# Kernel tuning notes

Measured on AMD Instinct MI355X. Metric: run time of the kernel, lower is better.

The kernel has to match this reference:

```python
import jax, jax.numpy as jnp
import numpy as np
from jax import lax

B, N, C = 4, 16384, 384  # C = 2*dim
DIM = C // 2
HH = WW = 128


def setup_inputs() -> dict:
    key = jax.random.key(0)
    ks = jax.random.split(key, 5)
    x = jax.random.normal(ks[0], (B, N, C), dtype=jnp.float32)
    conv_w = jax.random.normal(ks[1], (DIM, DIM, 4, 4), dtype=jnp.float32) * (1.0 / np.sqrt(DIM * 16))
    conv_b = jax.random.normal(ks[2], (DIM,), dtype=jnp.float32) * 0.02
    ln_w = jnp.ones((C,), dtype=jnp.float32)
    ln_b = jnp.zeros((C,), dtype=jnp.float32)
    proj_w = jax.random.normal(ks[3], (C, C), dtype=jnp.float32) * (1.0 / np.sqrt(C))
    proj_b = jax.random.normal(ks[4], (C,), dtype=jnp.float32) * 0.02
    return {"x": x, "conv_w": conv_w, "conv_b": conv_b, "ln_w": ln_w,
            "ln_b": ln_b, "proj_w": proj_w, "proj_b": proj_b, "H": HH, "W": WW}


def _csb_forward(x, conv_w, conv_b, ln_w, ln_b, proj_w, proj_b, H, W):
    Bb, Nn, Cc = x.shape
    d = Cc // 2
    x1 = x[..., :d]   # [B, N, d]
    x2 = x[..., d:]   # [B, N, d]

    # --- SpatialCorrection ---
    img = jnp.transpose(x2, (0, 2, 1)).reshape(Bb, d, H, W)  # NCHW
    y = lax.conv_general_dilated(img, conv_w, window_strides=(4, 4),
                                 padding='VALID',
                                 dimension_numbers=('NCHW', 'OIHW', 'NCHW'))
    y = y + conv_b[None, :, None, None]
    x2c = y.reshape(Bb, d, Nn // 16)                          # [B, d, M]
    gate = jax.nn.sigmoid(jnp.einsum('bnd,bdm->bnm', x1, x2c))  # [B, N, M]
    sp = jnp.einsum('bnm,bdm->bnd', gate, x2c)                 # [B, N, d]

    # --- ChannelCorrection ---
    att = jax.nn.softmax(jnp.einsum('bnd,bne->bde', x1, x2), axis=-2)  # [B, d, d], softmax over dim=-2
    ch = jnp.einsum('bnd,bde->bne', x2, att)                   # [B, N, d]

    # --- concat + LN + proj ---
    cat = jnp.concatenate([sp, ch], axis=-1)                   # [B, N, 2d]
    mu = jnp.mean(cat, axis=-1, keepdims=True)
    var = jnp.mean(jnp.square(cat - mu), axis=-1, keepdims=True)
    ln = (cat - mu) * lax.rsqrt(var + 1e-5) * ln_w + ln_b
    out = jnp.einsum('bnc,oc->bno', ln, proj_w) + proj_b
    return jnp.transpose(out, (0, 2, 1))                       # [B, 2d, N]


def reference(x, conv_w, conv_b, ln_w, ln_b, proj_w, proj_b, H, W):
    return _csb_forward(x, conv_w, conv_b, ln_w, ln_b, proj_w, proj_b, H, W)
```

## Files before the change

### kernel.cpp

```cpp
#include <hip/hip_runtime.h>

#define BB 4
#define NN 16384
#define CC 384
#define DD 192
#define MM 1024

typedef __attribute__((ext_vector_type(8))) short short8;
typedef __attribute__((ext_vector_type(4))) float f32x4;
typedef unsigned short u16;

__device__ __forceinline__ float4 ld4(const float* p) { return *reinterpret_cast<const float4*>(p); }

__device__ __forceinline__ u16 bf16r(float f) {
    unsigned int u = __float_as_uint(f);
    return (u16)((u + 0x7FFFu + ((u >> 16) & 1u)) >> 16);
}
__device__ __forceinline__ unsigned int pk2(float a, float b) {
    return (unsigned int)bf16r(a) | ((unsigned int)bf16r(b) << 16);
}
__device__ __forceinline__ short8 as_s8(uint4 v) {
    union { uint4 u; short8 s; } x; x.u = v; return x.s;
}
__device__ __forceinline__ f32x4 mfma16(short8 a, short8 b, f32x4 c) {
    return __builtin_amdgcn_mfma_f32_16x16x32_bf16(a, b, c, 0, 0, 0);
}
__device__ __forceinline__ void gload16(const void* g, void* l) {
    __builtin_amdgcn_global_load_lds(
        (const __attribute__((address_space(1))) void*)g,
        (__attribute__((address_space(3))) void*)l, 16, 0, 0);
}

__global__ __launch_bounds__(256) void k_prep(const float* __restrict__ pw, u16* __restrict__ pwb)
{
    int i = blockIdx.x * 256 + threadIdx.x;
    float4 v = ld4(&pw[i * 4]);
    uint2 o; o.x = pk2(v.x, v.y); o.y = pk2(v.z, v.w);
    reinterpret_cast<uint2*>(pwb)[i] = o;
}

__global__ __launch_bounds__(256) void k_prepw(const float* __restrict__ cw, u16* __restrict__ cwb)
{
    int idx = blockIdx.x * 256 + threadIdx.x;
    int k8 = idx / 192, o = idx % 192;
    int px = k8 / 24;
    int i0 = (k8 % 24) * 8;
    float f[8];
    #pragma unroll
    for (int e = 0; e < 8; ++e) f[e] = cw[(size_t)(o * 192 + i0 + e) * 16 + px];
    uint4 v = make_uint4(pk2(f[0], f[1]), pk2(f[2], f[3]), pk2(f[4], f[5]), pk2(f[6], f[7]));
    reinterpret_cast<uint4*>(cwb)[idx] = v;
}

__global__ __launch_bounds__(256) void k_conv(const float* __restrict__ x,
                                              const u16* __restrict__ cwb,
                                              float* __restrict__ Cp2)
{
    const int bid = blockIdx.x;
    const int s = bid >> 8, pt = bid & 255;
    const int b = pt >> 6;
    const int m0 = (pt & 63) * 16;
    const int P0 = pt * 16;
    const int t = threadIdx.x;
    const int l = t & 63, w = t >> 6;
    const int l15 = l & 15, l4 = l >> 4;
    const int o0 = w * 48;

    const int m = m0 + l15;
    const int ph = m >> 5, pw_ = m & 31;
    const float* xp = x + ((size_t)(b * NN) + ph * 512 + pw_ * 4) * CC + DD;

    f32x4 acc[3];
    #pragma unroll
    for (int ft = 0; ft < 3; ++ft) acc[ft] = (f32x4){0.f, 0.f, 0.f, 0.f};

    for (int kt = 0; kt < 48; ++kt) {
        const int px = s * 8 + kt / 6;
        const int i0 = (kt % 6) * 32;
        const int kh = px >> 2, kw = px & 3;
        const float* src = xp + (size_t)(kh * 128 + kw) * CC + i0 + l4 * 8;
        float4 v0 = ld4(src), v1 = ld4(src + 4);
        short8 av = as_s8(make_uint4(pk2(v0.x, v0.y), pk2(v0.z, v0.w), pk2(v1.x, v1.y), pk2(v1.z, v1.w)));
        const int k8g = px * 24 + (kt % 6) * 4 + l4;
        #pragma unroll
        for (int ft = 0; ft < 3; ++ft) {
            int o = o0 + ft * 16 + l15;
            short8 bv = as_s8(*reinterpret_cast<const uint4*>(cwb + (size_t)(k8g * 192 + o) * 8));
            acc[ft] = mfma16(av, bv, acc[ft]);
        }
    }
    #pragma unroll
    for (int ft = 0; ft < 3; ++ft)
        #pragma unroll
        for (int i = 0; i < 4; ++i)
            Cp2[(size_t)(s * 4096 + P0 + l4 * 4 + i) * 192 + o0 + ft * 16 + l15] = acc[ft][i];
}

__global__ __launch_bounds__(256) void k_convred(const float* __restrict__ Cp2,
                                                 const float* __restrict__ cb,
                                                 u16* __restrict__ x2cT,
                                                 u16* __restrict__ x2cM)
{
    __shared__ u16 T[64 * 194];
    const int bid = blockIdx.x;
    const int b = bid >> 4, mc = bid & 15;
    const int P0 = b * 1024 + mc * 64;
    const int t = threadIdx.x;
    #pragma unroll
    for (int j = 0; j < 12; ++j) {
        int idx = j * 256 + t;
        int row = idx / 48, c4 = idx % 48;
        float4 v0 = ld4(&Cp2[(size_t)(P0 + row) * 192 + c4 * 4]);
        float4 v1 = ld4(&Cp2[(size_t)(4096 + P0 + row) * 192 + c4 * 4]);
        float4 bb = ld4(&cb[c4 * 4]);
        float r0 = v0.x + v1.x + bb.x, r1 = v0.y + v1.y + bb.y;
        float r2 = v0.z + v1.z + bb.z, r3 = v0.w + v1.w + bb.w;
        u16 h0 = bf16r(r0), h1 = bf16r(r1), h2 = bf16r(r2), h3 = bf16r(r3);
        uint2 ov; ov.x = (unsigned int)h0 | ((unsigned int)h1 << 16);
        ov.y = (unsigned int)h2 | ((unsigned int)h3 << 16);
        *reinterpret_cast<uint2*>(x2cT + (size_t)(P0 + row) * 192 + c4 * 4) = ov;
        T[row * 194 + c4 * 4 + 0] = h0; T[row * 194 + c4 * 4 + 1] = h1;
        T[row * 194 + c4 * 4 + 2] = h2; T[row * 194 + c4 * 4 + 3] = h3;
    }
    __syncthreads();
    #pragma unroll
    for (int j = 0; j < 6; ++j) {
        int u = j * 256 + t;
        int o = u >> 3, m8 = (u & 7) * 8;
        unsigned int pk[4];
        #pragma unroll
        for (int q = 0; q < 4; ++q) {
            u16 a = T[(m8 + q * 2) * 194 + o];
            u16 c = T[(m8 + q * 2 + 1) * 194 + o];
            pk[q] = (unsigned int)a | ((unsigned int)c << 16);
        }
        *reinterpret_cast<uint4*>(x2cM + ((size_t)(b * DD + o) * MM) + mc * 64 + m8) =
            make_uint4(pk[0], pk[1], pk[2], pk[3]);
    }
}

__global__ __launch_bounds__(512) void k_S(const float* __restrict__ x, float* __restrict__ Sp,
                                           int KS, int nkt)
{
    __shared__ char LS[384 * 128];
    const int bid = blockIdx.x;
    const int b = bid / KS, ks = bid % KS;
    const int n0 = ks * (NN / KS);
    const int t = threadIdx.x;
    const int l = t & 63, w = t >> 6;
    const int rg = w >> 2, cs = w & 3;
    const int l15 = l & 15, l4 = l >> 4, key = (l15 & 7) << 4;

    const int c0 = (t & 127) * 3;
    const int krow = t >> 7;

    f32x4 acc[6][3];
    #pragma unroll
    for (int dt = 0; dt < 6; ++dt)
        #pragma unroll
        for (int et = 0; et < 3; ++et) acc[dt][et] = (f32x4){0.f, 0.f, 0.f, 0.f};

    for (int kt = 0; kt < nkt; ++kt) {
        __syncthreads();
        #pragma unroll
        for (int i = 0; i < 8; ++i) {
            int k = i * 4 + krow;
            const float* src = &x[(size_t)(b * NN + n0 + kt * 32 + k) * CC + c0];
            #pragma unroll
            for (int j = 0; j < 3; ++j) {
                int c = c0 + j;
                float v = src[j];
                u16 hi = bf16r(v);
                float hif = __uint_as_float(((unsigned int)hi) << 16);
                u16 lo = bf16r(v - hif);
                int base = c * 128;
                int ck = (c & 7) << 4;
                *reinterpret_cast<u16*>(LS + base + ((k * 2) ^ ck)) = hi;
                *reinterpret_cast<u16*>(LS + base + ((64 + k * 2) ^ ck)) = lo;
            }
        }
        __syncthreads();
        short8 bf[3][2];
        #pragma unroll
        for (int et = 0; et < 3; ++et) {
            int c = 192 + cs * 48 + et * 16 + l15;
            #pragma unroll
            for (int hl = 0; hl < 2; ++hl)
                bf[et][hl] = *reinterpret_cast<const short8*>(LS + c * 128 + ((hl * 64 + l4 * 16) ^ key));
        }
        #pragma unroll
        for (int dt = 0; dt < 6; ++dt) {
            int c = rg * 96 + dt * 16 + l15;
            short8 ah = *reinterpret_cast<const short8*>(LS + c * 128 + ((l4 * 16) ^ key));
            short8 al = *reinterpret_cast<const short8*>(LS + c * 128 + ((64 + l4 * 16) ^ key));
            #pragma unroll
            for (int et = 0; et < 3; ++et) {
                acc[dt][et] = mfma16(ah, bf[et][0], acc[dt][et]);
                acc[dt][et] = mfma16(ah, bf[et][1], acc[dt][et]);
                acc[dt][et] = mfma16(al, bf[et][0], acc[dt][et]);
            }
        }
    }
    float* dst = Sp + (size_t)(ks * BB + b) * 36864;
    #pragma unroll
    for (int dt = 0; dt < 6; ++dt)
        #pragma unroll
        for (int et = 0; et < 3; ++et) {
            int e = cs * 48 + et * 16 + l15;
            #pragma unroll
            for (int i = 0; i < 4; ++i) {
                int d = rg * 96 + dt * 16 + l4 * 4 + i;
                dst[d * 192 + e] = acc[dt][et][i];
            }
        }
}

__global__ __launch_bounds__(256) void k_sreduce(const float* __restrict__ Sp, float* __restrict__ S, int KS)
{
    int idx = blockIdx.x * 256 + threadIdx.x;
    int b = idx / 36864, de = idx % 36864;
    float s = 0.f;
    for (int p = 0; p < KS; ++p) s += Sp[(size_t)(p * BB + b) * 36864 + de];
    S[(size_t)b * 36864 + de] = s;
}

__global__ __launch_bounds__(64) void k_softmax(const float* __restrict__ S, u16* __restrict__ attT)
{
    const int bid = blockIdx.x;
    const int b = bid / 192, e = bid % 192;
    const int l = threadIdx.x;
    const float* Sb = S + (size_t)b * 36864 + e;
    float v0 = Sb[(size_t)(l * 3 + 0) * 192];
    float v1 = Sb[(size_t)(l * 3 + 1) * 192];
    float v2 = Sb[(size_t)(l * 3 + 2) * 192];
    float m = fmaxf(fmaxf(v0, v1), v2);
    #pragma unroll
    for (int s = 1; s < 64; s <<= 1) m = fmaxf(m, __shfl_xor(m, s, 64));
    v0 = __expf(v0 - m); v1 = __expf(v1 - m); v2 = __expf(v2 - m);
    float sum = v0 + v1 + v2;
    #pragma unroll
    for (int s = 1; s < 64; s <<= 1) sum += __shfl_xor(sum, s, 64);
    float inv = __fdividef(1.f, sum);
    u16* dst = attT + (size_t)b * 36864 + (size_t)e * 192 + l * 3;
    dst[0] = bf16r(v0 * inv); dst[1] = bf16r(v1 * inv); dst[2] = bf16r(v2 * inv);
}

#define KG_CT(p) ((p) * 24576)
#define KG_CM(p) ((p) * 24576 + 12288)
#define KG_GT 49152

__global__ __launch_bounds__(512, 2) void k_gate(
    const float* __restrict__ x, const u16* __restrict__ x2cT,
    const u16* __restrict__ x2cMp, const u16* __restrict__ attT,
    u16* __restrict__ cat, int half)
{
    __shared__ alignas(16) char LB[53248];
    const int t = threadIdx.x;
    const int l = t & 63, w = t >> 6;
    const int rg = w >> 1, cs = w & 1;
    const int b = blockIdx.x >> 7;
    const int nloc = (blockIdx.x & 127) << 6;
    const int n0 = half * 8192 + nloc;
    const int l15 = l & 15, l4 = l >> 4, key = (l15 & 7) << 4;
    const int key3 = (l15 & 3) << 4;
    const size_t xrow0 = (size_t)(b * NN + n0) * CC;
    const char* cbase = (const char*)x2cT;

    int goff[3], gmul[3];
    #pragma unroll
    for (int it = 0; it < 3; ++it) {
        int q = it * 8192 + w * 1024 + l * 16;
        if (q < 12288) {
            int m = q / 384, c = q % 384;
            goff[it] = b * 393216 + m * 384 + (c ^ ((m & 7) << 4));
            gmul[it] = 12288;
        } else {
            int qp = q - 12288;
            int r = qp >> 7, o = qp & 127;
            int op = o ^ ((r & 7) << 4);
            int d = r * 2 + (op >> 6);
            int m = (op & 63) >> 1;
            goff[it] = 1572864 + b * 393216 + d * 2048 + m * 2;
            gmul[it] = 64;
        }
    }
    (void)x2cMp;

    short8 ax1[6];
    {
        int row = rg * 16 + l15;
        const float* src = &x[xrow0 + (size_t)row * CC + l4 * 8];
        #pragma unroll
        for (int k = 0; k < 6; ++k) {
            float4 v0 = ld4(src + k * 32), v1 = ld4(src + k * 32 + 4);
            ax1[k] = as_s8(make_uint4(pk2(v0.x, v0.y), pk2(v0.z, v0.w), pk2(v1.x, v1.y), pk2(v1.z, v1.w)));
        }
    }

    #pragma unroll
    for (int it = 0; it < 3; ++it)
        gload16(cbase + goff[it], LB + it * 8192 + w * 1024);
    __syncthreads();

    f32x4 spa[6];
    #pragma unroll
    for (int nt = 0; nt < 6; ++nt) spa[nt] = (f32x4){0.f, 0.f, 0.f, 0.f};

    int p = 0;
    for (int mc = 0; mc < 32; ++mc) {
        if (mc < 31) {
            const int pn = p ^ 1;
            #pragma unroll
            for (int it = 0; it < 3; ++it)
                gload16(cbase + goff[it] + (mc + 1) * gmul[it],
                        LB + pn * 24576 + it * 8192 + w * 1024);
        }
        const char* bufCT = LB + KG_CT(p);
        const char* bufCM = LB + KG_CM(p);

        f32x4 cp = (f32x4){0.f, 0.f, 0.f, 0.f};
        #pragma unroll
        for (int kblk = 0; kblk < 6; ++kblk) {
            short8 a_ = *reinterpret_cast<const short8*>(
                bufCT + (cs * 16 + l15) * 384 + ((kblk * 64 + l4 * 16) ^ key));
            cp = mfma16(a_, ax1[kblk], cp);
        }
        {
            float g0 = __fdividef(1.f, 1.f + __expf(-cp[0]));
            float g1 = __fdividef(1.f, 1.f + __expf(-cp[1]));
            float g2 = __fdividef(1.f, 1.f + __expf(-cp[2]));
            float g3 = __fdividef(1.f, 1.f + __expf(-cp[3]));
            uint2 gv; gv.x = pk2(g0, g1); gv.y = pk2(g2, g3);
            *reinterpret_cast<uint2*>(LB + KG_GT + (rg * 16 + l15) * 64 +
                ((cs * 32 + l4 * 8) ^ key3)) = gv;
        }
        asm volatile("s_waitcnt lgkmcnt(0)" ::: "memory");
        __builtin_amdgcn_s_barrier();
        short8 ag = *reinterpret_cast<const short8*>(
            LB + KG_GT + (rg * 16 + l15) * 64 + ((l4 * 16) ^ key3));
        #pragma unroll
        for (int nt = 0; nt < 6; ++nt) {
            const int d = cs * 96 + nt * 16 + l15;
            const int rr = d >> 1;
            short8 bv = *reinterpret_cast<const short8*>(
                bufCM + rr * 128 + ((((d & 1) * 64) + l4 * 16) ^ ((rr & 7) << 4)));
            spa[nt] = mfma16(ag, bv, spa[nt]);
        }
        __syncthreads();
        p ^= 1;
    }

    short8 ax2[6];
    {
        int row = rg * 16 + l15;
        const float* src = &x[xrow0 + (size_t)row * CC + DD + l4 * 8];
        #pragma unroll
        for (int k = 0; k < 6; ++k) {
            float4 v0 = ld4(src + k * 32), v1 = ld4(src + k * 32 + 4);
            ax2[k] = as_s8(make_uint4(pk2(v0.x, v0.y), pk2(v0.z, v0.w), pk2(v1.x, v1.y), pk2(v1.z, v1.w)));
        }
    }
    f32x4 cha[6];
    #pragma unroll
    for (int nt = 0; nt < 6; ++nt) cha[nt] = (f32x4){0.f, 0.f, 0.f, 0.f};
    const u16* atb = attT + (size_t)b * 36864;
    #pragma unroll
    for (int nt = 0; nt < 6; ++nt) {
        int e = cs * 96 + nt * 16 + l15;
        #pragma unroll
        for (int k = 0; k < 6; ++k) {
            short8 bv = *reinterpret_cast<const short8*>(atb + (size_t)e * 192 + k * 32 + l4 * 8);
            cha[nt] = mfma16(ax2[k], bv, cha[nt]);
        }
    }

    #pragma unroll
    for (int nt = 0; nt < 6; ++nt) {
        int d = cs * 96 + nt * 16 + l15;
        #pragma unroll
        for (int i = 0; i < 4; ++i) {
            int row = rg * 16 + l4 * 4 + i;
            *reinterpret_cast<u16*>(LB + (row * 392 + d) * 2) = bf16r(spa[nt][i]);
            *reinterpret_cast<u16*>(LB + (row * 392 + DD + d) * 2) = bf16r(cha[nt][i]);
        }
    }
    __syncthreads();

    {
        const int row = t >> 3, q = t & 7;
        const size_t gbase = ((size_t)(b * 8192 + nloc + row)) * CC + q * 48;
        #pragma unroll
        for (int j = 0; j < 6; ++j) {
            uint4 v = *reinterpret_cast<const uint4*>(LB + (row * 392 + q * 48 + j * 8) * 2);
            *reinterpret_cast<uint4*>(cat + gbase + j * 8) = v;
        }
    }
}

#define PJ_PW 50176

__global__ __launch_bounds__(256, 2) void k_proj(
    const u16* __restrict__ cat, const float* __restrict__ lnw, const float* __restrict__ lnb,
    const u16* __restrict__ pwb, const float* __restrict__ pb,
    float* __restrict__ out, int half)
{
    __shared__ alignas(16) char LB[74752];
    const int t = threadIdx.x;
    const int l = t & 63, w = t >> 6;
    const int rg = w >> 1, cs = w & 1;
    const int b = blockIdx.x >> 7;
    const int nloc = (blockIdx.x & 127) << 6;
    const int n0 = half * 8192 + nloc;
    const int l15 = l & 15, l4 = l >> 4;

    #pragma unroll
    for (int j = 0; j < 12; ++j) {
        int u = j * 256 + t;
        int row = u / 48, c8 = (u % 48) * 8;
        uint4 v = *reinterpret_cast<const uint4*>(cat + ((size_t)(b * 8192 + nloc + row)) * CC + c8);
        *reinterpret_cast<uint4*>(LB + (row * 392 + c8) * 2) = v;
    }
    __syncthreads();

    {
        const int rowL = t >> 2, q = t & 3;
        char* lbase = LB + (rowL * 392 + q * 96) * 2;
        float s = 0.f, ss = 0.f;
        #pragma unroll
        for (int u = 0; u < 12; ++u) {
            uint4 pv = *reinterpret_cast<const uint4*>(lbase + u * 16);
            const unsigned int* pu = &pv.x;
            #pragma unroll
            for (int h = 0; h < 4; ++h) {
                float f0 = __uint_as_float(pu[h] << 16);
                float f1 = __uint_as_float(pu[h] & 0xFFFF0000u);
                s += f0 + f1; ss += f0 * f0 + f1 * f1;
            }
        }
        s += __shfl_xor(s, 1, 4);  s += __shfl_xor(s, 2, 4);
        ss += __shfl_xor(ss, 1, 4); ss += __shfl_xor(ss, 2, 4);
        float mu = s * (1.f / 384.f);
        float var = ss * (1.f / 384.f) - mu * mu;
        float rs = rsqrtf(var + 1e-5f);
        const int c0 = q * 96;
        #pragma unroll
        for (int u = 0; u < 12; ++u) {
            uint4 pv = *reinterpret_cast<const uint4*>(lbase + u * 16);
            const unsigned int* pu = &pv.x;
            float4 w0 = ld4(&lnw[c0 + u * 8]), w1 = ld4(&lnw[c0 + u * 8 + 4]);
            float4 b0 = ld4(&lnb[c0 + u * 8]), b1 = ld4(&lnb[c0 + u * 8 + 4]);
            float f[8];
            #pragma unroll
            for (int h = 0; h < 4; ++h) {
                f[2 * h]     = __uint_as_float(pu[h] << 16);
                f[2 * h + 1] = __uint_as_float(pu[h] & 0xFFFF0000u);
            }
            f[0] = (f[0] - mu) * rs * w0.x + b0.x; f[1] = (f[1] - mu) * rs * w0.y + b0.y;
            f[2] = (f[2] - mu) * rs * w0.z + b0.z; f[3] = (f[3] - mu) * rs * w0.w + b0.w;
            f[4] = (f[4] - mu) * rs * w1.x + b1.x; f[5] = (f[5] - mu) * rs * w1.y + b1.y;
            f[6] = (f[6] - mu) * rs * w1.z + b1.z; f[7] = (f[7] - mu) * rs * w1.w + b1.w;
            *reinterpret_cast<uint4*>(lbase + u * 16) =
                make_uint4(pk2(f[0], f[1]), pk2(f[2], f[3]), pk2(f[4], f[5]), pk2(f[6], f[7]));
        }
    }

    f32x4 pacc[2][12];
    #pragma unroll
    for (int rt = 0; rt < 2; ++rt)
        #pragma unroll
        for (int nt = 0; nt < 12; ++nt) pacc[rt][nt] = (f32x4){0.f, 0.f, 0.f, 0.f};
    for (int kt = 0; kt < 12; ++kt) {
        __syncthreads();
        #pragma unroll
        for (int j = 0; j < 6; ++j) {
            int u = j * 256 + t;
            int o = u >> 2, c8 = (u & 3) * 8;
            uint4 pv = *reinterpret_cast<const uint4*>(pwb + (size_t)o * CC + kt * 32 + c8);
            *reinterpret_cast<uint4*>(LB + PJ_PW + (((o * 32 + c8) * 2) ^ ((o & 7) << 4))) = pv;
        }
        __syncthreads();
        short8 av[2];
        #pragma unroll
        for (int rt = 0; rt < 2; ++rt) {
            int row = rg * 32 + rt * 16 + l15;
            av[rt] = *reinterpret_cast<const short8*>(LB + (row * 392 + kt * 32 + l4 * 8) * 2);
        }
        #pragma unroll
        for (int nt = 0; nt < 12; ++nt) {
            int o = cs * 192 + nt * 16 + l15;
            short8 bv = *reinterpret_cast<const short8*>(
                LB + PJ_PW + (((o * 32 + l4 * 8) * 2) ^ ((o & 7) << 4)));
            pacc[0][nt] = mfma16(av[0], bv, pacc[0][nt]);
            pacc[1][nt] = mfma16(av[1], bv, pacc[1][nt]);
        }
    }
    __syncthreads();

    float* T = reinterpret_cast<float*>(LB + PJ_PW);
    for (int os = 0; os < 6; ++os) {
        if (cs == (os >= 3 ? 1 : 0)) {
            const int nt0 = (os % 3) * 4;
            #pragma unroll
            for (int nt = 0; nt < 4; ++nt) {
                int o_l = nt * 16 + l15;
                float bias = pb[os * 64 + o_l];
                #pragma unroll
                for (int rt = 0; rt < 2; ++rt)
                    #pragma unroll
                    for (int i = 0; i < 4; ++i)
                        T[o_l * 68 + rg * 32 + rt * 16 + l4 * 4 + i] = pacc[rt][nt0 + nt][i] + bias;
            }
        }
        __syncthreads();
        {
            const int o_l = t >> 2, nq = t & 3;
            const size_t gbase = (size_t)(b * CC + os * 64 + o_l) * NN + n0 + nq * 16;
            #pragma unroll
            for (int j = 0; j < 4; ++j) {
                float4 v = *reinterpret_cast<const float4*>(&T[o_l * 68 + nq * 16 + j * 4]);
                *reinterpret_cast<float4*>(&out[gbase + j * 4]) = v;
            }
        }
        __syncthreads();
    }
}

extern "C" void kernel_launch(void* const* d_in, const int* in_sizes, int n_in,
                              void* d_out, int out_size, void* d_ws, size_t ws_size,
                              hipStream_t stream)
{
    (void)in_sizes; (void)n_in; (void)out_size;
    const float* x   = (const float*)d_in[0];
    const float* cw  = (const float*)d_in[1];
    const float* cb  = (const float*)d_in[2];
    const float* lnw = (const float*)d_in[3];
    const float* lnb = (const float*)d_in[4];
    const float* pwm = (const float*)d_in[5];
    const float* pbv = (const float*)d_in[6];
    float* out = (float*)d_out;
    char* w0 = (char*)d_ws;

    u16* x2cT = (u16*)(w0);
    u16* x2cM = (u16*)(w0 + 1572864);
    u16* attT = (u16*)(w0 + 3145728);
    u16* pwb  = (u16*)(w0 + 3440640);
    u16* cwb  = (u16*)(w0 + 3735552);
    float* Cp2 = (float*)(w0 + 4915200);
    float* Sp  = (float*)(w0 + 11206656);
    u16*   cat = (u16*)(w0 + 4915200);
    float* Sf  = (float*)(w0 + 30081024);

    int KS = 32;
    if (ws_size >= (size_t)68419584) {
        KS = 64;
        Sp = (float*)(w0 + 30670848);
    }
    const int nkt = (NN / KS) / 32;

    hipLaunchKernelGGL(k_prep,    dim3(144),      dim3(256), 0, stream, pwm, pwb);
    hipLaunchKernelGGL(k_prepw,   dim3(288),      dim3(256), 0, stream, cw, cwb);
    hipLaunchKernelGGL(k_conv,    dim3(512),      dim3(256), 0, stream, x, cwb, Cp2);
    hipLaunchKernelGGL(k_convred, dim3(64),       dim3(256), 0, stream, Cp2, cb, x2cT, x2cM);
    hipLaunchKernelGGL(k_S,       dim3(BB * KS),  dim3(512), 0, stream, x, Sp, KS, nkt);
    hipLaunchKernelGGL(k_sreduce, dim3(576),      dim3(256), 0, stream, Sp, Sf, KS);
    hipLaunchKernelGGL(k_softmax, dim3(BB * 192), dim3(64),  0, stream, Sf, attT);
    for (int h = 0; h < 2; ++h) {
        hipLaunchKernelGGL(k_gate, dim3(512), dim3(512), 0, stream, x, x2cT, x2cM, attT, cat, h);
        hipLaunchKernelGGL(k_proj, dim3(512), dim3(256), 0, stream, cat, lnw, lnb, pwb, pbv, out, h);
    }
}
```

Measured before the change: 339.9 us.

## Fuse gate and projection kernels into one, keeping cat tile in LDS

```diff
diff --git a/kernel.cpp b/kernel.cpp
--- a/kernel.cpp
+++ b/kernel.cpp
@@ -245,24 +245,23 @@
     dst[0] = bf16r(v0 * inv); dst[1] = bf16r(v1 * inv); dst[2] = bf16r(v2 * inv);
 }
 
-#define KG_CT(p) ((p) * 24576)
-#define KG_CM(p) ((p) * 24576 + 12288)
-#define KG_GT 49152
-
-__global__ __launch_bounds__(512, 2) void k_gate(
+#define KF_CAT 0
+#define KF_PW  50176
+
+__global__ __launch_bounds__(512, 4) void k_fused2(
     const float* __restrict__ x, const u16* __restrict__ x2cT,
-    const u16* __restrict__ x2cMp, const u16* __restrict__ attT,
-    u16* __restrict__ cat, int half)
-{
-    __shared__ alignas(16) char LB[53248];
+    const u16* __restrict__ attT,
+    const float* __restrict__ lnw, const float* __restrict__ lnb,
+    const u16* __restrict__ pwb, const float* __restrict__ pb,
+    float* __restrict__ out)
+{
+    __shared__ alignas(16) char LB[74752];
     const int t = threadIdx.x;
     const int l = t & 63, w = t >> 6;
     const int rg = w >> 1, cs = w & 1;
-    const int b = blockIdx.x >> 7;
-    const int nloc = (blockIdx.x & 127) << 6;
-    const int n0 = half * 8192 + nloc;
+    const int b = blockIdx.x >> 8;
+    const int n0 = (blockIdx.x & 255) << 6;
     const int l15 = l & 15, l4 = l >> 4, key = (l15 & 7) << 4;
-    const int key3 = (l15 & 3) << 4;
     const size_t xrow0 = (size_t)(b * NN + n0) * CC;
     const char* cbase = (const char*)x2cT;
 
@@ -284,7 +283,6 @@
             gmul[it] = 64;
         }
     }
-    (void)x2cMp;
 
     short8 ax1[6];
     {
@@ -315,29 +313,42 @@
                 gload16(cbase + goff[it] + (mc + 1) * gmul[it],
                         LB + pn * 24576 + it * 8192 + w * 1024);
         }
-        const char* bufCT = LB + KG_CT(p);
-        const char* bufCM = LB + KG_CM(p);
-
-        f32x4 cp = (f32x4){0.f, 0.f, 0.f, 0.f};
+        const char* bufCT = LB + p * 24576;
+        const char* bufCM = bufCT + 12288;
+
+        f32x4 cp0 = (f32x4){0.f, 0.f, 0.f, 0.f};
+        f32x4 cp1 = (f32x4){0.f, 0.f, 0.f, 0.f};
         #pragma unroll
         for (int kblk = 0; kblk < 6; ++kblk) {
-            short8 a_ = *reinterpret_cast<const short8*>(
-                bufCT + (cs * 16 + l15) * 384 + ((kblk * 64 + l4 * 16) ^ key));
-            cp = mfma16(a_, ax1[kblk], cp);
-        }
+            short8 a0 = *reinterpret_cast<const short8*>(
+                bufCT + l15 * 384 + ((kblk * 64 + l4 * 16) ^ key));
+            short8 a1 = *reinterpret_cast<const short8*>(
+                bufCT + (16 + l15) * 384 + ((kblk * 64 + l4 * 16) ^ key));
+            cp0 = mfma16(a0, ax1[kblk], cp0);
+            cp1 = mfma16(a1, ax1[kblk], cp1);
+        }
+        unsigned int pA0[2], pA1[2];
         {
-            float g0 = __fdividef(1.f, 1.f + __expf(-cp[0]));
-            float g1 = __fdividef(1.f, 1.f + __expf(-cp[1]));
-            float g2 = __fdividef(1.f, 1.f + __expf(-cp[2]));
-            float g3 = __fdividef(1.f, 1.f + __expf(-cp[3]));
-            uint2 gv; gv.x = pk2(g0, g1); gv.y = pk2(g2, g3);
-            *reinterpret_cast<uint2*>(LB + KG_GT + (rg * 16 + l15) * 64 +
-                ((cs * 32 + l4 * 8) ^ key3)) = gv;
-        }
-        asm volatile("s_waitcnt lgkmcnt(0)" ::: "memory");
-        __builtin_amdgcn_s_barrier();
-        short8 ag = *reinterpret_cast<const short8*>(
-            LB + KG_GT + (rg * 16 + l15) * 64 + ((l4 * 16) ^ key3));
+            float g0 = __fdividef(1.f, 1.f + __expf(-cp0[0]));
+            float g1 = __fdividef(1.f, 1.f + __expf(-cp0[1]));
+            float g2 = __fdividef(1.f, 1.f + __expf(-cp0[2]));
+            float g3 = __fdividef(1.f, 1.f + __expf(-cp0[3]));
+            pA0[0] = pk2(g0, g1); pA0[1] = pk2(g2, g3);
+            g0 = __fdividef(1.f, 1.f + __expf(-cp1[0]));
+            g1 = __fdividef(1.f, 1.f + __expf(-cp1[1]));
+            g2 = __fdividef(1.f, 1.f + __expf(-cp1[2]));
+            g3 = __fdividef(1.f, 1.f + __expf(-cp1[3]));
+            pA1[0] = pk2(g0, g1); pA1[1] = pk2(g2, g3);
+        }
+        unsigned int W[4];
+        #pragma unroll
+        for (int qp = 0; qp < 4; ++qp) {
+            int sl = ((((l4 << 1) + (qp >> 1)) & 3) << 4) + l15;
+            int a0 = __shfl((int)pA0[qp & 1], sl, 64);
+            int a1 = __shfl((int)pA1[qp & 1], sl, 64);
+            W[qp] = (l4 & 2) ? (unsigned int)a1 : (unsigned int)a0;
+        }
+        short8 ag = as_s8(make_uint4(W[0], W[1], W[2], W[3]));
         #pragma unroll
         for (int nt = 0; nt < 6; ++nt) {
             const int d = cs * 96 + nt * 16 + l15;
@@ -387,47 +398,11 @@
     __syncthreads();
 
     {
-        const int row = t >> 3, q = t & 7;
-        const size_t gbase = ((size_t)(b * 8192 + nloc + row)) * CC + q * 48;
-        #pragma unroll
-        for (int j = 0; j < 6; ++j) {
-            uint4 v = *reinterpret_cast<const uint4*>(LB + (row * 392 + q * 48 + j * 8) * 2);
-            *reinterpret_cast<uint4*>(cat + gbase + j * 8) = v;
-        }
-    }
-}
-
-#define PJ_PW 50176
-
-__global__ __launch_bounds__(256, 2) void k_proj(
-    const u16* __restrict__ cat, const float* __restrict__ lnw, const float* __restrict__ lnb,
-    const u16* __restrict__ pwb, const float* __restrict__ pb,
-    float* __restrict__ out, int half)
-{
-    __shared__ alignas(16) char LB[74752];
-    const int t = threadIdx.x;
-    const int l = t & 63, w = t >> 6;
-    const int rg = w >> 1, cs = w & 1;
-    const int b = blockIdx.x >> 7;
-    const int nloc = (blockIdx.x & 127) << 6;
-    const int n0 = half * 8192 + nloc;
-    const int l15 = l & 15, l4 = l >> 4;
-
-    #pragma unroll
-    for (int j = 0; j < 12; ++j) {
-        int u = j * 256 + t;
-        int row = u / 48, c8 = (u % 48) * 8;
-        uint4 v = *reinterpret_cast<const uint4*>(cat + ((size_t)(b * 8192 + nloc + row)) * CC + c8);
-        *reinterpret_cast<uint4*>(LB + (row * 392 + c8) * 2) = v;
-    }
-    __syncthreads();
-
-    {
-        const int rowL = t >> 2, q = t & 3;
-        char* lbase = LB + (rowL * 392 + q * 96) * 2;
+        const int rowL = t >> 3, q = t & 7;
+        char* lbase = LB + rowL * 784 + q * 96;
         float s = 0.f, ss = 0.f;
         #pragma unroll
-        for (int u = 0; u < 12; ++u) {
+        for (int u = 0; u < 6; ++u) {
             uint4 pv = *reinterpret_cast<const uint4*>(lbase + u * 16);
             const unsigned int* pu = &pv.x;
             #pragma unroll
@@ -437,14 +412,14 @@
                 s += f0 + f1; ss += f0 * f0 + f1 * f1;
             }
         }
-        s += __shfl_xor(s, 1, 4);  s += __shfl_xor(s, 2, 4);
-        ss += __shfl_xor(ss, 1, 4); ss += __shfl_xor(ss, 2, 4);
+        s += __shfl_xor(s, 1, 8);  s += __shfl_xor(s, 2, 8);  s += __shfl_xor(s, 4, 8);
+        ss += __shfl_xor(ss, 1, 8); ss += __shfl_xor(ss, 2, 8); ss += __shfl_xor(ss, 4, 8);
         float mu = s * (1.f / 384.f);
         float var = ss * (1.f / 384.f) - mu * mu;
         float rs = rsqrtf(var + 1e-5f);
-        const int c0 = q * 96;
-        #pragma unroll
-        for (int u = 0; u < 12; ++u) {
+        const int c0 = q * 48;
+        #pragma unroll
+        for (int u = 0; u < 6; ++u) {
             uint4 pv = *reinterpret_cast<const uint4*>(lbase + u * 16);
             const unsigned int* pu = &pv.x;
             float4 w0 = ld4(&lnw[c0 + u * 8]), w1 = ld4(&lnw[c0 + u * 8 + 4]);
@@ -464,39 +439,32 @@
         }
     }
 
-    f32x4 pacc[2][12];
-    #pragma unroll
-    for (int rt = 0; rt < 2; ++rt)
-        #pragma unroll
-        for (int nt = 0; nt < 12; ++nt) pacc[rt][nt] = (f32x4){0.f, 0.f, 0.f, 0.f};
+    f32x4 pacc[12];
+    #pragma unroll
+    for (int nt = 0; nt < 12; ++nt) pacc[nt] = (f32x4){0.f, 0.f, 0.f, 0.f};
     for (int kt = 0; kt < 12; ++kt) {
         __syncthreads();
         #pragma unroll
-        for (int j = 0; j < 6; ++j) {
-            int u = j * 256 + t;
+        for (int j = 0; j < 3; ++j) {
+            int u = j * 512 + t;
             int o = u >> 2, c8 = (u & 3) * 8;
             uint4 pv = *reinterpret_cast<const uint4*>(pwb + (size_t)o * CC + kt * 32 + c8);
-            *reinterpret_cast<uint4*>(LB + PJ_PW + (((o * 32 + c8) * 2) ^ ((o & 7) << 4))) = pv;
-        }
-        __syncthreads();
-        short8 av[2];
-        #pragma unroll
-        for (int rt = 0; rt < 2; ++rt) {
-            int row = rg * 32 + rt * 16 + l15;
-            av[rt] = *reinterpret_cast<const short8*>(LB + (row * 392 + kt * 32 + l4 * 8) * 2);
-        }
+            *reinterpret_cast<uint4*>(LB + KF_PW + (((o * 32 + c8) * 2) ^ ((o & 7) << 4))) = pv;
+        }
+        __syncthreads();
+        short8 av = *reinterpret_cast<const short8*>(
+            LB + ((rg * 16 + l15) * 392 + kt * 32 + l4 * 8) * 2);
         #pragma unroll
         for (int nt = 0; nt < 12; ++nt) {
             int o = cs * 192 + nt * 16 + l15;
             short8 bv = *reinterpret_cast<const short8*>(
-                LB + PJ_PW + (((o * 32 + l4 * 8) * 2) ^ ((o & 7) << 4)));
-            pacc[0][nt] = mfma16(av[0], bv, pacc[0][nt]);
-            pacc[1][nt] = mfma16(av[1], bv, pacc[1][nt]);
+                LB + KF_PW + (((o * 32 + l4 * 8) * 2) ^ ((o & 7) << 4)));
+            pacc[nt] = mfma16(av, bv, pacc[nt]);
         }
     }
     __syncthreads();
 
-    float* T = reinterpret_cast<float*>(LB + PJ_PW);
+    float* T = reinterpret_cast<float*>(LB + KF_PW);
     for (int os = 0; os < 6; ++os) {
         if (cs == (os >= 3 ? 1 : 0)) {
             const int nt0 = (os % 3) * 4;
@@ -505,21 +473,18 @@
                 int o_l = nt * 16 + l15;
                 float bias = pb[os * 64 + o_l];
                 #pragma unroll
-                for (int rt = 0; rt < 2; ++rt)
-                    #pragma unroll
-                    for (int i = 0; i < 4; ++i)
-                        T[o_l * 68 + rg * 32 + rt * 16 + l4 * 4 + i] = pacc[rt][nt0 + nt][i] + bias;
+                for (int i = 0; i < 4; ++i)
+                    T[o_l * 68 + rg * 16 + l4 * 4 + i] = pacc[nt0 + nt][i] + bias;
             }
         }
         __syncthreads();
         {
-            const int o_l = t >> 2, nq = t & 3;
-            const size_t gbase = (size_t)(b * CC + os * 64 + o_l) * NN + n0 + nq * 16;
-            #pragma unroll
-            for (int j = 0; j < 4; ++j) {
-                float4 v = *reinterpret_cast<const float4*>(&T[o_l * 68 + nq * 16 + j * 4]);
-                *reinterpret_cast<float4*>(&out[gbase + j * 4]) = v;
-            }
+            const int o_l = t >> 3, nq = t & 7;
+            const size_t gbase = (size_t)(b * CC + os * 64 + o_l) * NN + n0 + nq * 8;
+            float4 v0 = *reinterpret_cast<const float4*>(&T[o_l * 68 + nq * 8]);
+            float4 v1 = *reinterpret_cast<const float4*>(&T[o_l * 68 + nq * 8 + 4]);
+            *reinterpret_cast<float4*>(&out[gbase]) = v0;
+            *reinterpret_cast<float4*>(&out[gbase + 4]) = v1;
         }
         __syncthreads();
     }
@@ -547,7 +512,6 @@
     u16* cwb  = (u16*)(w0 + 3735552);
     float* Cp2 = (float*)(w0 + 4915200);
     float* Sp  = (float*)(w0 + 11206656);
-    u16*   cat = (u16*)(w0 + 4915200);
     float* Sf  = (float*)(w0 + 30081024);
 
     int KS = 32;
@@ -564,8 +528,6 @@
     hipLaunchKernelGGL(k_S,       dim3(BB * KS),  dim3(512), 0, stream, x, Sp, KS, nkt);
     hipLaunchKernelGGL(k_sreduce, dim3(576),      dim3(256), 0, stream, Sp, Sf, KS);
     hipLaunchKernelGGL(k_softmax, dim3(BB * 192), dim3(64),  0, stream, Sf, attT);
-    for (int h = 0; h < 2; ++h) {
-        hipLaunchKernelGGL(k_gate, dim3(512), dim3(512), 0, stream, x, x2cT, x2cM, attT, cat, h);
-        hipLaunchKernelGGL(k_proj, dim3(512), dim3(256), 0, stream, cat, lnw, lnb, pwb, pbv, out, h);
-    }
-}
+    hipLaunchKernelGGL(k_fused2,  dim3(1024),     dim3(512), 0, stream,
+                       x, x2cT, attT, lnw, lnb, pwb, pbv, out);
+}
```

Result: faster. 319.0 us (-6.2%).
